# Performance work log

Measured on AMD Instinct MI355X. Metric: run time of the kernel, lower is better.

## Reference

```python
import jax, jax.numpy as jnp
import numpy as np

N, C, H = 16384, 16, 64
K = 9  # n_neighbors + 1 (self included, as in torch_cluster knn(x, x, k+1))
UPDATE_RATE = 0.001


def setup_inputs() -> dict:
    key = jax.random.key(0)
    k1, k2, k3 = jax.random.split(key, 3)
    x = jax.random.normal(k1, (N, C), dtype=jnp.float32)
    # Glorot-ish init for GCN layer weights
    W1 = jax.random.normal(k2, (C, H), dtype=jnp.float32) * (1.0 / np.sqrt(C))
    b1 = jnp.zeros((H,), dtype=jnp.float32)
    W2 = jax.random.normal(k3, (H, C), dtype=jnp.float32) * (1.0 / np.sqrt(H))
    b2 = jnp.zeros((C,), dtype=jnp.float32)
    return {"x": x, "W1": W1, "b1": b1, "W2": W2, "b2": b2, "n_steps": 4}


def _knn_idx(coords):
    # coords: [N, 2]; brute-force squared distances, top-K nearest (incl. self)
    sq = jnp.sum(coords * coords, axis=1)                  # [N]
    d2 = sq[:, None] + sq[None, :] - 2.0 * (coords @ coords.T)  # [N, N]
    _, idx = jax.lax.top_k(-d2, K)                         # [N, K]
    return idx


def _npa_step(x, W1, b1, W2, b2):
    idx = _knn_idx(x[:, :2])                 # rebuild kNN graph from coords
    agg1 = jnp.mean(x[idx], axis=1)          # [N, C] gather + mean aggregate
    h = jax.nn.relu(agg1 @ W1 + b1)          # GCN layer 1
    agg2 = jnp.mean(h[idx], axis=1)          # [N, H]
    update = agg2 @ W2 + b2                  # GCN layer 2 (no activation)
    return x + update * UPDATE_RATE


def reference(x, W1, b1, W2, b2, n_steps):
    for _ in range(n_steps):
        x = _npa_step(x, W1, b1, W2, b2)
    return x
```

## Files before the change

kernel.cpp:

```cpp
#include <hip/hip_runtime.h>
#include <hip/hip_bf16.h>


#define NPTS 16384
#define CDIM 16
#define HDIM 64
#define KNN 9
#define G 128
#define NCELL (G * G)
#define HCELL (12.0f / 128.0f)
#define RMAX_MAIN 8
#define MARGIN 1e-4f

__device__ __forceinline__ unsigned sortable_f32(float f) {
    unsigned u = __float_as_uint(f);
    return (u & 0x80000000u) ? ~u : (u | 0x80000000u);
}
__device__ __forceinline__ int cellcoord(float v) {
    int c = (int)floorf((v + 6.0f) * ((float)G / 12.0f));
    return min(G - 1, max(0, c));
}
__device__ __forceinline__ unsigned long long shfl_xor_u64(unsigned long long v, int off) {
    int lo = __shfl_xor((int)(v & 0xffffffffu), off);
    int hi = __shfl_xor((int)(v >> 32), off);
    return ((unsigned long long)(unsigned)hi << 32) | (unsigned)lo;
}
__device__ __forceinline__ float ref_d2(float qx, float qy, float qsq, float cx, float cy, float csq) {
    float dot = __fadd_rn(__fmul_rn(qx, cx), __fmul_rn(qy, cy));
    return __fsub_rn(__fadd_rn(qsq, csq), __fadd_rn(dot, dot));
}
#define INSERT9(a, k)                                            \
    {                                                            \
        unsigned long long _k = (k);                             \
        _Pragma("unroll")                                        \
        for (int _s = 0; _s < 9; ++_s) {                         \
            unsigned long long _lo = (_k < a[_s]) ? _k : a[_s];  \
            unsigned long long _hi = (_k < a[_s]) ? a[_s] : _k;  \
            a[_s] = _lo; _k = _hi;                               \
        }                                                        \
    }

__device__ __forceinline__ bool done_check_sq(const unsigned long long a[9],
                                              float qx, float qy, int cx, int cy, int r) {
    float xlo = -6.0f + (float)(cx - r) * HCELL;
    float xhi = -6.0f + (float)(cx + r + 1) * HCELL;
    float ylo = -6.0f + (float)(cy - r) * HCELL;
    float yhi = -6.0f + (float)(cy + r + 1) * HCELL;
    float slack = fminf(fminf(qx - xlo, xhi - qx), fminf(qy - ylo, yhi - qy));
    slack = fmaxf(slack, 0.0f);
    float bf = __fsub_rn(__fmul_rn(slack, slack), MARGIN);
    unsigned bu = sortable_f32(bf);
    int c9 = 0;
#pragma unroll
    for (int s = 0; s < 9; ++s) c9 += ((unsigned)(a[s] >> 32) <= bu) ? 1 : 0;
    c9 += __shfl_xor(c9, 1);
    c9 += __shfl_xor(c9, 2);
    c9 += __shfl_xor(c9, 4);
    c9 += __shfl_xor(c9, 8);
    c9 += __shfl_xor(c9, 16);
    return c9 >= 9;
}

__device__ __forceinline__ void merge32_pop9(unsigned long long a[9], unsigned long long m[9]) {
#pragma unroll
    for (int round = 0; round < 9; ++round) {
        unsigned long long g = a[0];
        unsigned long long o = shfl_xor_u64(g, 1);  if (o < g) g = o;
        o = shfl_xor_u64(g, 2);  if (o < g) g = o;
        o = shfl_xor_u64(g, 4);  if (o < g) g = o;
        o = shfl_xor_u64(g, 8);  if (o < g) g = o;
        o = shfl_xor_u64(g, 16); if (o < g) g = o;
        if (a[0] == g) {
#pragma unroll
            for (int s = 0; s < 8; ++s) a[s] = a[s + 1];
            a[8] = ~0ull;
        }
        m[round] = g;
    }
}

__global__ __launch_bounds__(256) void zero_kernel(int* __restrict__ cnt) {
    int i = blockIdx.x * 256 + threadIdx.x;
    if (i < NCELL) cnt[i] = 0;
}

__global__ __launch_bounds__(256) void pack_hist_kernel(const float* __restrict__ x,
                                                        float4* __restrict__ cand,
                                                        int* __restrict__ cellOf,
                                                        int* __restrict__ cnt) {
    int i = blockIdx.x * 256 + threadIdx.x;
    if (i >= NPTS) return;
    float xx = x[i * CDIM + 0];
    float yy = x[i * CDIM + 1];
    float sq = __fadd_rn(__fmul_rn(xx, xx), __fmul_rn(yy, yy));
    cand[i] = make_float4(xx, yy, sq, 0.0f);
    int c = cellcoord(yy) * G + cellcoord(xx);
    cellOf[i] = c;
    atomicAdd(&cnt[c], 1);
}

__global__ __launch_bounds__(1024) void scan_kernel(const int* __restrict__ cnt,
                                                    int* __restrict__ cellStart,
                                                    int* __restrict__ ctr,
                                                    int* __restrict__ flcnt) {
    __shared__ int wsum[16];
    const int tid = threadIdx.x;
    const int lane = tid & 63;
    const int wid = tid >> 6;
    if (tid == 0) *flcnt = 0;
    const int4* c4 = (const int4*)cnt;
    int4* cs4 = (int4*)cellStart;
    int4* ct4 = (int4*)ctr;
    const int b4 = tid * 4;
    int s = 0;
#pragma unroll
    for (int j = 0; j < 4; ++j) {
        int4 t = c4[b4 + j];
        s += t.x + t.y + t.z + t.w;
    }
    int inc = s;
#pragma unroll
    for (int off = 1; off < 64; off <<= 1) {
        int o = __shfl_up(inc, off);
        if (lane >= off) inc += o;
    }
    if (lane == 63) wsum[wid] = inc;
    __syncthreads();
    if (wid == 0 && lane < 16) {
        int v = wsum[lane];
        int iv = v;
#pragma unroll
        for (int off = 1; off < 16; off <<= 1) {
            int o = __shfl_up(iv, off);
            if (lane >= off) iv += o;
        }
        wsum[lane] = iv - v;
    }
    __syncthreads();
    int run = wsum[wid] + (inc - s);
#pragma unroll
    for (int j = 0; j < 4; ++j) {
        int4 t = c4[b4 + j];
        int4 o;
        o.x = run; run += t.x;
        o.y = run; run += t.y;
        o.z = run; run += t.z;
        o.w = run; run += t.w;
        cs4[b4 + j] = o;
        ct4[b4 + j] = o;
    }
    if (tid == 1023) cellStart[NCELL] = run;
}

__global__ __launch_bounds__(256) void scatter_kernel(const float4* __restrict__ cand,
                                                      const int* __restrict__ cellOf,
                                                      int* __restrict__ ctr,
                                                      float4* __restrict__ sorted,
                                                      int* __restrict__ cnt) {
    int i = blockIdx.x * 256 + threadIdx.x;
    if (i < NPTS) {
        float4 c = cand[i];
        int pos = atomicAdd(&ctr[cellOf[i]], 1);
        sorted[pos] = make_float4(c.x, c.y, c.z, __int_as_float(i));
        if (i < NCELL / 4) ((int4*)cnt)[i] = make_int4(0, 0, 0, 0);
    }
}

__global__ __launch_bounds__(256) void knn_grid_kernel(const float4* __restrict__ sorted,
                                                       const int* __restrict__ cellStart,
                                                       int* __restrict__ idxb,
                                                       int* __restrict__ fl,
                                                       int* __restrict__ flcnt) {
    const int wl = threadIdx.x & 63;
    const int sl = wl & 31;
    const int base = wl & ~31;
    const int t = blockIdx.x * 8 + (threadIdx.x >> 5);

    float4 qd = sorted[t];
    const float qx = qd.x, qy = qd.y, qsq = qd.z;
    const int qid = __float_as_int(qd.w);
    const int cx = cellcoord(qx), cy = cellcoord(qy);

    unsigned long long a[9];
#pragma unroll
    for (int s = 0; s < 9; ++s) a[s] = ~0ull;

    {
        const int x0 = max(cx - 1, 0), x1 = min(cx + 1, G - 1);
        int sv = 0, ev = 0;
        if (sl < 3) {
            int yy = cy - 1 + sl;
            if (yy >= 0 && yy < G) {
                sv = cellStart[yy * G + x0];
                ev = cellStart[yy * G + x1 + 1];
            }
        }
        int s0 = __shfl(sv, base + 0), e0 = __shfl(ev, base + 0);
        int s1 = __shfl(sv, base + 1), e1 = __shfl(ev, base + 1);
        int s2 = __shfl(sv, base + 2), e2 = __shfl(ev, base + 2);
        const int L0 = e0 - s0;
        const int L01 = L0 + (e1 - s1);
        const int M = L01 + (e2 - s2);

        for (int g2 = sl; g2 < M; g2 += 32) {
            int p = (g2 < L0) ? (s0 + g2) : (g2 < L01 ? (s1 + g2 - L0) : (s2 + g2 - L01));
            float4 pt = sorted[p];
            float d = ref_d2(qx, qy, qsq, pt.x, pt.y, pt.z);
            unsigned long long key =
                ((unsigned long long)sortable_f32(d) << 32) | (unsigned)__float_as_int(pt.w);
            if (key < a[8]) INSERT9(a, key);
        }
    }

    bool done = done_check_sq(a, qx, qy, cx, cy, 1);

#pragma unroll 1
    for (int r = 2; r <= RMAX_MAIN; ++r) {
        if (__all(done)) break;
        if (!done) {
            const int twor = 2 * r;
            for (int i = sl; i < 8 * r; i += 32) {
                int side = (i >= twor) + (i >= 2 * twor) + (i >= 3 * twor);
                int off = i - side * twor;
                int xx, yy;
                if (side == 0)      { yy = cy - r; xx = cx - r + off; }
                else if (side == 1) { xx = cx + r; yy = cy - r + off; }
                else if (side == 2) { yy = cy + r; xx = cx + r - off; }
                else                { xx = cx - r; yy = cy + r - off; }
                if (xx < 0 || xx >= G || yy < 0 || yy >= G) continue;
                int cell = yy * G + xx;
                int s = cellStart[cell];
                int e = cellStart[cell + 1];
                for (int p = s; p < e; ++p) {
                    float4 pt = sorted[p];
                    float d = ref_d2(qx, qy, qsq, pt.x, pt.y, pt.z);
                    unsigned long long key =
                        ((unsigned long long)sortable_f32(d) << 32) | (unsigned)__float_as_int(pt.w);
                    if (key < a[8]) INSERT9(a, key);
                }
            }
            done = done_check_sq(a, qx, qy, cx, cy, r);
        }
    }

    if (done) {
        unsigned long long m[9];
        merge32_pop9(a, m);
        if (sl < 9) idxb[qid * KNN + sl] = (int)(m[sl] & 0xffffffffu);
    } else if (sl == 0) {
        int pos = atomicAdd(flcnt, 1);
        fl[pos] = qid;
    }
}

__global__ __launch_bounds__(1024) void knn_brute_kernel(const float4* __restrict__ cand,
                                                         const int* __restrict__ fl,
                                                         const int* __restrict__ flcnt,
                                                         int* __restrict__ idxb) {
    __shared__ unsigned long long wtop[16][9];
    const int tid = threadIdx.x;
    const int lane = tid & 63;
    const int wid = tid >> 6;
    const int nf = *flcnt;

    for (int fi = blockIdx.x; fi < nf; fi += gridDim.x) {
        const int qid = fl[fi];
        float4 qc = cand[qid];
        const float qx = qc.x, qy = qc.y, qsq = qc.z;

        unsigned long long a[9];
#pragma unroll
        for (int s = 0; s < 9; ++s) a[s] = ~0ull;

#pragma unroll
        for (int j = 0; j < 4; ++j) {
            const int b = j * 4096 + tid;
            float4 c0 = cand[b];
            float4 c1 = cand[b + 1024];
            float4 c2 = cand[b + 2048];
            float4 c3 = cand[b + 3072];
#define PROC(cc, kk)                                                                   \
            {                                                                          \
                float d = ref_d2(qx, qy, qsq, (cc).x, (cc).y, (cc).z);                 \
                unsigned long long key =                                               \
                    ((unsigned long long)sortable_f32(d) << 32) | (unsigned)(b + (kk) * 1024); \
                if (key < a[8]) INSERT9(a, key);                                       \
            }
            PROC(c0, 0) PROC(c1, 1) PROC(c2, 2) PROC(c3, 3)
#undef PROC
        }

#pragma unroll
        for (int round = 0; round < 9; ++round) {
            unsigned long long g = a[0];
#pragma unroll
            for (int off = 32; off >= 1; off >>= 1) {
                unsigned long long o = shfl_xor_u64(g, off);
                if (o < g) g = o;
            }
            if (a[0] == g) {
#pragma unroll
                for (int s = 0; s < 8; ++s) a[s] = a[s + 1];
                a[8] = ~0ull;
            }
            if (lane == 0) wtop[wid][round] = g;
        }
        __syncthreads();

        if (wid == 0) {
            unsigned long long b0 = (lane < 144)       ? wtop[lane / 9][lane % 9] : ~0ull;
            unsigned long long b1 = (lane + 64 < 144)  ? wtop[(lane + 64) / 9][(lane + 64) % 9] : ~0ull;
            unsigned long long b2 = (lane + 128 < 144) ? wtop[(lane + 128) / 9][(lane + 128) % 9] : ~0ull;
            { unsigned long long t = min(b0, b1), u = max(b0, b1); b0 = t; b1 = u; }
            { unsigned long long t = min(b1, b2), u = max(b1, b2); b1 = t; b2 = u; }
            { unsigned long long t = min(b0, b1), u = max(b0, b1); b0 = t; b1 = u; }
#pragma unroll
            for (int round = 0; round < 9; ++round) {
                unsigned long long g = b0;
#pragma unroll
                for (int off = 32; off >= 1; off >>= 1) {
                    unsigned long long o = shfl_xor_u64(g, off);
                    if (o < g) g = o;
                }
                if (b0 == g) { b0 = b1; b1 = b2; b2 = ~0ull; }
                if (lane == 0) idxb[qid * KNN + round] = (int)(g & 0xffffffffu);
            }
        }
        __syncthreads();
    }
}

__global__ __launch_bounds__(256) void gcn1_kernel(const float* __restrict__ x,
                                                   const int* __restrict__ idxb,
                                                   const float* __restrict__ W1,
                                                   const float* __restrict__ b1,
                                                   float* __restrict__ h) {
    const int lane = threadIdx.x & 63;
    int node = blockIdx.x * 4 + (threadIdx.x >> 6);
    const int n = __builtin_amdgcn_readfirstlane(node);

    const int kg = lane >> 4;
    const int c = lane & 15;

    float agg = 0.0f;
#pragma unroll
    for (int j = 0; j < 3; ++j) {
        int kk = kg + 4 * j;
        if (kk < KNN) {
            int nb = idxb[n * KNN + kk];
            agg += x[nb * CDIM + c];
        }
    }
    agg += __shfl_xor(agg, 16);
    agg += __shfl_xor(agg, 32);
    agg = agg / 9.0f;

    float hv = b1[lane];
#pragma unroll
    for (int mm = 0; mm < CDIM; mm++) {
        float am = __shfl(agg, mm);
        hv = fmaf(am, W1[mm * HDIM + lane], hv);
    }
    h[n * HDIM + lane] = fmaxf(hv, 0.0f);
}

__global__ __launch_bounds__(256) void gcn2_kernel(const float* __restrict__ xold,
                                                   const float* __restrict__ h,
                                                   const int* __restrict__ idxb,
                                                   const float* __restrict__ W2,
                                                   const float* __restrict__ b2,
                                                   float* __restrict__ xnew,
                                                   float4* __restrict__ cand,
                                                   int* __restrict__ cellOf,
                                                   int* __restrict__ cnt) {
    const int lane = threadIdx.x & 63;
    int node = blockIdx.x * 4 + (threadIdx.x >> 6);
    const int n = __builtin_amdgcn_readfirstlane(node);

    float ag = 0.0f;
#pragma unroll
    for (int k = 0; k < KNN; k++) {
        int nb = idxb[n * KNN + k];
        ag += h[nb * HDIM + lane];
    }
    ag = ag / 9.0f;

    const int c = lane & (CDIM - 1);
    float o = b2[c];
#pragma unroll
    for (int mm = 0; mm < HDIM; mm++) {
        float am = __shfl(ag, mm);
        o = fmaf(am, W2[mm * CDIM + c], o);
    }
    float xv = 0.0f;
    if (lane < CDIM) {
        xv = __fadd_rn(xold[n * CDIM + lane], __fmul_rn(o, 0.001f));
        xnew[n * CDIM + lane] = xv;
    }
    float xx = __shfl(xv, 0);
    float yy = __shfl(xv, 1);
    if (lane == 0) {
        float sq = __fadd_rn(__fmul_rn(xx, xx), __fmul_rn(yy, yy));
        cand[n] = make_float4(xx, yy, sq, 0.0f);
        int cell = cellcoord(yy) * G + cellcoord(xx);
        cellOf[n] = cell;
        atomicAdd(&cnt[cell], 1);
    }
}

extern "C" void kernel_launch(void* const* d_in, const int* in_sizes, int n_in,
                              void* d_out, int out_size, void* d_ws, size_t ws_size,
                              hipStream_t stream) {
    const float* x0 = (const float*)d_in[0];
    const float* W1 = (const float*)d_in[1];
    const float* b1 = (const float*)d_in[2];
    const float* W2 = (const float*)d_in[3];
    const float* b2 = (const float*)d_in[4];

    char* w = (char*)d_ws;
    float4* cand      = (float4*)(w + 0);
    float4* sorted    = (float4*)(w + 262144);
    int*    cellOf    = (int*)   (w + 524288);
    int*    cnt       = (int*)   (w + 589824);
    int*    flcnt     = (int*)   (w + 851968);
    int*    cellStart = (int*)   (w + 852032);
    int*    ctr       = (int*)   (w + 1114240);
    int*    fl        = (int*)   (w + 1376384);
    int*    idxb      = (int*)   (w + 1441920);
    float*  xA        = (float*) (w + 2031744);
    float*  xB        = (float*) (w + 3080320);
    float*  hbuf      = (float*) (w + 4128896);
    const float* xin = x0;
    float* bufs[2] = { xA, xB };

    zero_kernel<<<NCELL / 256, 256, 0, stream>>>(cnt);
    pack_hist_kernel<<<NPTS / 256, 256, 0, stream>>>(x0, cand, cellOf, cnt);

    for (int s = 0; s < 4; s++) {
        float* xout = (s == 3) ? (float*)d_out : bufs[s & 1];

        scan_kernel<<<1, 1024, 0, stream>>>(cnt, cellStart, ctr, flcnt);
        scatter_kernel<<<NPTS / 256, 256, 0, stream>>>(cand, cellOf, ctr, sorted, cnt);
        knn_grid_kernel<<<NPTS / 8, 256, 0, stream>>>(sorted, cellStart, idxb, fl, flcnt);
        knn_brute_kernel<<<64, 1024, 0, stream>>>(cand, fl, flcnt, idxb);
        gcn1_kernel<<<NPTS / 4, 256, 0, stream>>>(xin, idxb, W1, b1, hbuf);
        gcn2_kernel<<<NPTS / 4, 256, 0, stream>>>(xin, hbuf, idxb, W2, b2, xout, cand, cellOf, cnt);

        xin = xout;
    }
}
```

Measured before the change: 330.3 us.

## Fuse kNN search with GCN layer 1 and inline brute-force fallback

The grid kNN kernel now also computes the layer-1 aggregation and the W1 projection, writing h directly from the merged neighbour list. This removes the separate gcn1 launch and the idxb round trip. The separate brute-force fallback kernel and its failure-list bookkeeping are gone. Queries not resolved within the search radius now scan all points inside the 32-lane group. That removes two launches per step, but a rare unresolved query stalls its wave on a full serial scan instead of using a wide 1024-thread block.

```diff
diff --git a/kernel.cpp b/kernel.cpp
--- a/kernel.cpp
+++ b/kernel.cpp
@@ -101,13 +101,11 @@
 
 __global__ __launch_bounds__(1024) void scan_kernel(const int* __restrict__ cnt,
                                                     int* __restrict__ cellStart,
-                                                    int* __restrict__ ctr,
-                                                    int* __restrict__ flcnt) {
+                                                    int* __restrict__ ctr) {
     __shared__ int wsum[16];
     const int tid = threadIdx.x;
     const int lane = tid & 63;
     const int wid = tid >> 6;
-    if (tid == 0) *flcnt = 0;
     const int4* c4 = (const int4*)cnt;
     int4* cs4 = (int4*)cellStart;
     int4* ct4 = (int4*)ctr;
@@ -166,11 +164,13 @@
     }
 }
 
-__global__ __launch_bounds__(256) void knn_grid_kernel(const float4* __restrict__ sorted,
+__global__ __launch_bounds__(256) void knn_gcn1_kernel(const float4* __restrict__ sorted,
                                                        const int* __restrict__ cellStart,
+                                                       const float* __restrict__ xin,
+                                                       const float* __restrict__ W1,
+                                                       const float* __restrict__ b1,
                                                        int* __restrict__ idxb,
-                                                       int* __restrict__ fl,
-                                                       int* __restrict__ flcnt) {
+                                                       float* __restrict__ h) {
     const int wl = threadIdx.x & 63;
     const int sl = wl & 31;
     const int base = wl & ~31;
@@ -184,6 +184,14 @@
     unsigned long long a[9];
 #pragma unroll
     for (int s = 0; s < 9; ++s) a[s] = ~0ull;
+
+#define PROCK(cc)                                                                        \
+    {                                                                                    \
+        float d = ref_d2(qx, qy, qsq, (cc).x, (cc).y, (cc).z);                           \
+        unsigned long long key =                                                         \
+            ((unsigned long long)sortable_f32(d) << 32) | (unsigned)__float_as_int((cc).w); \
+        if (key < a[8]) INSERT9(a, key);                                                 \
+    }
 
     {
         const int x0 = max(cx - 1, 0), x1 = min(cx + 1, G - 1);
@@ -205,10 +213,7 @@
         for (int g2 = sl; g2 < M; g2 += 32) {
             int p = (g2 < L0) ? (s0 + g2) : (g2 < L01 ? (s1 + g2 - L0) : (s2 + g2 - L01));
             float4 pt = sorted[p];
-            float d = ref_d2(qx, qy, qsq, pt.x, pt.y, pt.z);
-            unsigned long long key =
-                ((unsigned long long)sortable_f32(d) << 32) | (unsigned)__float_as_int(pt.w);
-            if (key < a[8]) INSERT9(a, key);
+            PROCK(pt)
         }
     }
 
@@ -233,135 +238,56 @@
                 int e = cellStart[cell + 1];
                 for (int p = s; p < e; ++p) {
                     float4 pt = sorted[p];
-                    float d = ref_d2(qx, qy, qsq, pt.x, pt.y, pt.z);
-                    unsigned long long key =
-                        ((unsigned long long)sortable_f32(d) << 32) | (unsigned)__float_as_int(pt.w);
-                    if (key < a[8]) INSERT9(a, key);
+                    PROCK(pt)
                 }
             }
             done = done_check_sq(a, qx, qy, cx, cy, r);
         }
     }
 
-    if (done) {
-        unsigned long long m[9];
-        merge32_pop9(a, m);
-        if (sl < 9) idxb[qid * KNN + sl] = (int)(m[sl] & 0xffffffffu);
-    } else if (sl == 0) {
-        int pos = atomicAdd(flcnt, 1);
-        fl[pos] = qid;
-    }
-}
-
-__global__ __launch_bounds__(1024) void knn_brute_kernel(const float4* __restrict__ cand,
-                                                         const int* __restrict__ fl,
-                                                         const int* __restrict__ flcnt,
-                                                         int* __restrict__ idxb) {
-    __shared__ unsigned long long wtop[16][9];
-    const int tid = threadIdx.x;
-    const int lane = tid & 63;
-    const int wid = tid >> 6;
-    const int nf = *flcnt;
-
-    for (int fi = blockIdx.x; fi < nf; fi += gridDim.x) {
-        const int qid = fl[fi];
-        float4 qc = cand[qid];
-        const float qx = qc.x, qy = qc.y, qsq = qc.z;
-
-        unsigned long long a[9];
+    if (!done) {
 #pragma unroll
         for (int s = 0; s < 9; ++s) a[s] = ~0ull;
-
-#pragma unroll
-        for (int j = 0; j < 4; ++j) {
-            const int b = j * 4096 + tid;
-            float4 c0 = cand[b];
-            float4 c1 = cand[b + 1024];
-            float4 c2 = cand[b + 2048];
-            float4 c3 = cand[b + 3072];
-#define PROC(cc, kk)                                                                   \
-            {                                                                          \
-                float d = ref_d2(qx, qy, qsq, (cc).x, (cc).y, (cc).z);                 \
-                unsigned long long key =                                               \
-                    ((unsigned long long)sortable_f32(d) << 32) | (unsigned)(b + (kk) * 1024); \
-                if (key < a[8]) INSERT9(a, key);                                       \
+#pragma unroll 1
+        for (int p0 = 0; p0 < NPTS; p0 += 128) {
+            float4 c0 = sorted[p0 + sl];
+            float4 c1 = sorted[p0 + sl + 32];
+            float4 c2 = sorted[p0 + sl + 64];
+            float4 c3 = sorted[p0 + sl + 96];
+            PROCK(c0) PROCK(c1) PROCK(c2) PROCK(c3)
+        }
+    }
+#undef PROCK
+
+    unsigned long long m[9];
+    merge32_pop9(a, m);
+    if (sl < 9) idxb[qid * KNN + sl] = (int)(m[sl] & 0xffffffffu);
+
+    {
+        const int c = sl & 15;
+        const int half = sl >> 4;
+        float sum = 0.0f;
+#pragma unroll
+        for (int k = 0; k < KNN; ++k) {
+            if ((k & 1) == half) {
+                int nb = (int)(m[k] & 0xffffffffu);
+                sum += xin[nb * CDIM + c];
             }
-            PROC(c0, 0) PROC(c1, 1) PROC(c2, 2) PROC(c3, 3)
-#undef PROC
-        }
-
-#pragma unroll
-        for (int round = 0; round < 9; ++round) {
-            unsigned long long g = a[0];
-#pragma unroll
-            for (int off = 32; off >= 1; off >>= 1) {
-                unsigned long long o = shfl_xor_u64(g, off);
-                if (o < g) g = o;
-            }
-            if (a[0] == g) {
-#pragma unroll
-                for (int s = 0; s < 8; ++s) a[s] = a[s + 1];
-                a[8] = ~0ull;
-            }
-            if (lane == 0) wtop[wid][round] = g;
-        }
-        __syncthreads();
-
-        if (wid == 0) {
-            unsigned long long b0 = (lane < 144)       ? wtop[lane / 9][lane % 9] : ~0ull;
-            unsigned long long b1 = (lane + 64 < 144)  ? wtop[(lane + 64) / 9][(lane + 64) % 9] : ~0ull;
-            unsigned long long b2 = (lane + 128 < 144) ? wtop[(lane + 128) / 9][(lane + 128) % 9] : ~0ull;
-            { unsigned long long t = min(b0, b1), u = max(b0, b1); b0 = t; b1 = u; }
-            { unsigned long long t = min(b1, b2), u = max(b1, b2); b1 = t; b2 = u; }
-            { unsigned long long t = min(b0, b1), u = max(b0, b1); b0 = t; b1 = u; }
-#pragma unroll
-            for (int round = 0; round < 9; ++round) {
-                unsigned long long g = b0;
-#pragma unroll
-                for (int off = 32; off >= 1; off >>= 1) {
-                    unsigned long long o = shfl_xor_u64(g, off);
-                    if (o < g) g = o;
-                }
-                if (b0 == g) { b0 = b1; b1 = b2; b2 = ~0ull; }
-                if (lane == 0) idxb[qid * KNN + round] = (int)(g & 0xffffffffu);
-            }
-        }
-        __syncthreads();
-    }
-}
-
-__global__ __launch_bounds__(256) void gcn1_kernel(const float* __restrict__ x,
-                                                   const int* __restrict__ idxb,
-                                                   const float* __restrict__ W1,
-                                                   const float* __restrict__ b1,
-                                                   float* __restrict__ h) {
-    const int lane = threadIdx.x & 63;
-    int node = blockIdx.x * 4 + (threadIdx.x >> 6);
-    const int n = __builtin_amdgcn_readfirstlane(node);
-
-    const int kg = lane >> 4;
-    const int c = lane & 15;
-
-    float agg = 0.0f;
-#pragma unroll
-    for (int j = 0; j < 3; ++j) {
-        int kk = kg + 4 * j;
-        if (kk < KNN) {
-            int nb = idxb[n * KNN + kk];
-            agg += x[nb * CDIM + c];
-        }
-    }
-    agg += __shfl_xor(agg, 16);
-    agg += __shfl_xor(agg, 32);
-    agg = agg / 9.0f;
-
-    float hv = b1[lane];
-#pragma unroll
-    for (int mm = 0; mm < CDIM; mm++) {
-        float am = __shfl(agg, mm);
-        hv = fmaf(am, W1[mm * HDIM + lane], hv);
-    }
-    h[n * HDIM + lane] = fmaxf(hv, 0.0f);
+        }
+        sum += __shfl_xor(sum, 16);
+        float agg = sum / 9.0f;
+
+        float hv0 = b1[sl];
+        float hv1 = b1[sl + 32];
+#pragma unroll
+        for (int mm = 0; mm < CDIM; ++mm) {
+            float am = __shfl(agg, base + mm);
+            hv0 = fmaf(am, W1[mm * HDIM + sl], hv0);
+            hv1 = fmaf(am, W1[mm * HDIM + sl + 32], hv1);
+        }
+        h[qid * HDIM + sl] = fmaxf(hv0, 0.0f);
+        h[qid * HDIM + sl + 32] = fmaxf(hv1, 0.0f);
+    }
 }
 
 __global__ __launch_bounds__(256) void gcn2_kernel(const float* __restrict__ xold,
@@ -422,14 +348,13 @@
     float4* sorted    = (float4*)(w + 262144);
     int*    cellOf    = (int*)   (w + 524288);
     int*    cnt       = (int*)   (w + 589824);
-    int*    flcnt     = (int*)   (w + 851968);
     int*    cellStart = (int*)   (w + 852032);
     int*    ctr       = (int*)   (w + 1114240);
-    int*    fl        = (int*)   (w + 1376384);
     int*    idxb      = (int*)   (w + 1441920);
     float*  xA        = (float*) (w + 2031744);
     float*  xB        = (float*) (w + 3080320);
     float*  hbuf      = (float*) (w + 4128896);
+
     const float* xin = x0;
     float* bufs[2] = { xA, xB };
 
@@ -439,11 +364,9 @@
     for (int s = 0; s < 4; s++) {
         float* xout = (s == 3) ? (float*)d_out : bufs[s & 1];
 
-        scan_kernel<<<1, 1024, 0, stream>>>(cnt, cellStart, ctr, flcnt);
+        scan_kernel<<<1, 1024, 0, stream>>>(cnt, cellStart, ctr);
         scatter_kernel<<<NPTS / 256, 256, 0, stream>>>(cand, cellOf, ctr, sorted, cnt);
-        knn_grid_kernel<<<NPTS / 8, 256, 0, stream>>>(sorted, cellStart, idxb, fl, flcnt);
-        knn_brute_kernel<<<64, 1024, 0, stream>>>(cand, fl, flcnt, idxb);
-        gcn1_kernel<<<NPTS / 4, 256, 0, stream>>>(xin, idxb, W1, b1, hbuf);
+        knn_gcn1_kernel<<<NPTS / 8, 256, 0, stream>>>(sorted, cellStart, xin, W1, b1, idxb, hbuf);
         gcn2_kernel<<<NPTS / 4, 256, 0, stream>>>(xin, hbuf, idxb, W2, b2, xout, cand, cellOf, cnt);
 
         xin = xout;
```

After: 693.3 us. 2.1x slower.
